# Kernel tuning notes

Hardware: AMD Instinct MI355X
Metric: run time of the kernel (lower is better)

## Reference

```python
import jax, jax.numpy as jnp
import numpy as np

BLOCK = 64
THRESH = 0.95
EPS = 1e-8


def setup_inputs() -> dict:
    key = jax.random.key(0)
    kq, kk, kv = jax.random.split(key, 3)
    S, D = 4096, 128
    q = jax.random.normal(kq, (S, D), dtype=jnp.float32)
    k = jax.random.normal(kk, (S, D), dtype=jnp.float32)
    v = jax.random.normal(kv, (S, D), dtype=jnp.float32)
    return {"q": q, "k": k, "v": v}


def reference(q, k, v):
    S, D = q.shape
    nb = S // BLOCK
    qb = q.reshape(nb, BLOCK, D)
    kb = k.reshape(nb, BLOCK, D)
    vb = v.reshape(nb, BLOCK, D)
    # all block-pair scores: [nb_q, nb_k, BLOCK_q, BLOCK_k]
    scores = jnp.einsum('ibd,jcd->ijbc', qb, kb)
    m = jnp.max(scores, axis=-1, keepdims=True)
    e = jnp.exp(scores - m)
    s = jnp.sum(e, axis=-1, keepdims=True)  # per-block-pair softmax denominator
    # top-p truncation mask: sort descending, cumsum, threshold
    srt = jnp.sort(e, axis=-1)[..., ::-1]
    cum = jnp.cumsum(srt, axis=-1)
    mask = cum < THRESH * s
    # NOTE: faithful to original — mask (in sorted order) is applied to the
    # UNSORTED exp_scores, exactly as the torch code does (indices unused).
    em = e * mask
    em = em / (jnp.sum(em, axis=-1, keepdims=True) + EPS)
    # accumulate over key blocks j (per-pair normalized weights, summed)
    out = jnp.einsum('ijbc,jcd->ibd', em, vb)
    return out.reshape(S, D)
```

## Files before the change

### kernel.cpp

```cpp
#include <hip/hip_runtime.h>
#include <cstdint>
#include <cstddef>


#define SEQ   4096
#define DIM   128
#define BLK   64
#define NB    (SEQ / BLK)
#define NJG   16
#define JPB   (NB / NJG)
#define NT    256
#define PSTR  12288
#define THRESH 0.95f
#define EPSF   1e-8f

typedef __attribute__((ext_vector_type(8))) _Float16 f16x8;
typedef __attribute__((ext_vector_type(4))) float    f32x4;

#define MFMAH(a, b, c) __builtin_amdgcn_mfma_f32_16x16x32_f16((a), (b), (c), 0, 0, 0)

union UH4 { uint2 u; _Float16 h[4]; };
union UH8 { uint4 u; f16x8 v; };

__device__ __forceinline__ void gll16(const uint* g, uint* l) {
  __builtin_amdgcn_global_load_lds(
      (const __attribute__((address_space(1))) void*)g,
      (__attribute__((address_space(3))) void*)l, 16, 0, 0);
}

__global__ __launch_bounds__(NT, 4) void eco_prep_kernel(
    const float* __restrict__ K, const float* __restrict__ V,
    uint* __restrict__ P, float* __restrict__ O) {
  const int tid  = threadIdx.x;
  const int b    = blockIdx.x;
  const int jb   = b >> 2;
  const int part = b & 3;

  {
    float4 z = {0.f, 0.f, 0.f, 0.f};
    float4* op = (float4*)O;
#pragma unroll
    for (int it = 0; it < 2; ++it) op[b * 512 + it * NT + tid] = z;
  }

  {
    const float4* gk = (const float4*)(K + (size_t)jb * BLK * DIM);
    uint* dst = P + (size_t)jb * PSTR;
#pragma unroll
    for (int it = 0; it < 2; ++it) {
      int f = part * 512 + it * NT + tid;
      int r = f >> 5, c4 = f & 31;
      float4 x = gk[f];
      float xs[4] = {x.x, x.y, x.z, x.w};
      UH4 uh, ur;
#pragma unroll
      for (int e = 0; e < 4; ++e) {
        float v = xs[e];
        _Float16 h = (_Float16)v;
        uh.h[e] = h;
        ur.h[e] = (_Float16)(v - (float)h);
      }
      uint off = (uint)r * 64u + (((uint)(c4 >> 1) ^ (uint)(r & 15)) << 2) +
                 (uint)((c4 & 1) << 1);
      *(uint2*)&dst[off]        = uh.u;
      *(uint2*)&dst[4096 + off] = ur.u;
    }
  }

  {
    const float* gv = V + (size_t)jb * BLK * DIM;
    uint4* dv = (uint4*)(P + (size_t)jb * PSTR + 8192);
    int idx = part * 256 + tid;
    int ch = idx >> 7, d = idx & 127;
    UH8 u;
#pragma unroll
    for (int j = 0; j < 8; ++j)
      u.v[j] = (_Float16)gv[(ch * 8 + j) * DIM + d];
    dv[idx] = u.u;
  }
}

#define CE(x, y, dmax) { float _hi = fmaxf((x), (y)); float _lo = fminf((x), (y)); \
                         (x) = (dmax) ? _hi : _lo; (y) = (dmax) ? _lo : _hi; }

__global__ __launch_bounds__(NT, 4) void eco_attn_kernel(
    const float* __restrict__ Q, const uint* __restrict__ P,
    float* __restrict__ O) {
  __shared__ __align__(16) uint sK[8192];
  __shared__ __align__(16) uint sW[2048];

  const int tid  = threadIdx.x;
  const int ib   = blockIdx.y;
  const int jg   = blockIdx.x;
  const int lane = tid & 63;
  const int wv   = tid >> 6;
  const int quad = lane >> 4;
  const int l16  = lane & 15;
  const int q4   = quad << 2;

  uint* sWw = sW + wv * 512;

  f16x8 qh[4], qr[4];
  {
    const float* qp = Q + (size_t)(ib * BLK + wv * 16 + l16) * DIM + quad * 8;
#pragma unroll
    for (int ks = 0; ks < 4; ++ks) {
      float4 x0 = *(const float4*)(qp + ks * 32);
      float4 x1 = *(const float4*)(qp + ks * 32 + 4);
      float xs[8] = {x0.x, x0.y, x0.z, x0.w, x1.x, x1.y, x1.z, x1.w};
      f16x8 h8, r8;
#pragma unroll
      for (int e = 0; e < 8; ++e) {
        float v = xs[e];
        _Float16 h = (_Float16)v;
        h8[e] = h;
        r8[e] = (_Float16)(v - (float)h);
      }
      qh[ks] = h8; qr[ks] = r8;
    }
  }

  const f32x4 zf = {0.f, 0.f, 0.f, 0.f};
  f32x4 pv[8];
#pragma unroll
  for (int i = 0; i < 8; ++i) pv[i] = zf;

  {
    const uint* gsrc = P + (size_t)(jg * JPB) * PSTR;
#pragma unroll
    for (int it = 0; it < 8; ++it) {
      int idx = (it * NT + tid) << 2;
      gll16(gsrc + idx, sK + idx);
    }
  }

  for (int jj = 0; jj < JPB; ++jj) {
    const int jb = jg * JPB + jj;
    __syncthreads();

    f32x4 ah[4], ar[4];
#pragma unroll
    for (int nt = 0; nt < 4; ++nt) { ah[nt] = zf; ar[nt] = zf; }
#pragma unroll
    for (int nt = 0; nt < 4; ++nt) {
      const int rB = nt * 16 + l16;
      const uint rowoff = (uint)rB * 64u;
      const uint swk = (uint)(rB & 15);
#pragma unroll
      for (int ks = 0; ks < 4; ++ks) {
        uint off = rowoff + ((((uint)(ks * 4 + quad)) ^ swk) << 2);
        f16x8 bh = *(const f16x8*)&sK[off];
        f16x8 br = *(const f16x8*)&sK[4096 + off];
        ah[nt] = MFMAH(bh, qh[ks], ah[nt]);
        ar[nt] = MFMAH(br, qh[ks], ar[nt]);
        ar[nt] = MFMAH(bh, qr[ks], ar[nt]);
      }
    }
    __syncthreads();

    if (jj + 1 < JPB) {
      const uint* gsrc = P + (size_t)(jb + 1) * PSTR;
#pragma unroll
      for (int it = 0; it < 8; ++it) {
        int idx = (it * NT + tid) << 2;
        gll16(gsrc + idx, sK + idx);
      }
    }

    {
      float a[16], e[16];
#pragma unroll
      for (int nt = 0; nt < 4; ++nt) {
        f32x4 s = ah[nt] + ar[nt];
#pragma unroll
        for (int rg = 0; rg < 4; ++rg) a[nt * 4 + rg] = s[rg];
      }
      float mt[8];
#pragma unroll
      for (int i = 0; i < 8; ++i) mt[i] = fmaxf(a[i], a[i + 8]);
#pragma unroll
      for (int w2 = 4; w2 >= 1; w2 >>= 1)
#pragma unroll
        for (int i = 0; i < w2; ++i) mt[i] = fmaxf(mt[i], mt[i + w2]);
      float m = mt[0];
      m = fmaxf(m, __shfl_xor(m, 16, 64));
      m = fmaxf(m, __shfl_xor(m, 32, 64));
#pragma unroll
      for (int i = 0; i < 16; ++i) { a[i] = __expf(a[i] - m); e[i] = a[i]; }
      float st[8];
#pragma unroll
      for (int i = 0; i < 8; ++i) st[i] = a[i] + a[i + 8];
#pragma unroll
      for (int w2 = 4; w2 >= 1; w2 >>= 1)
#pragma unroll
        for (int i = 0; i < w2; ++i) st[i] += st[i + w2];
      float sr = st[0];
      sr += __shfl_xor(sr, 16, 64);
      sr += __shfl_xor(sr, 32, 64);
      const float T = THRESH * sr;

      const int s = quad;
#pragma unroll
      for (int k2 = 2; k2 <= 8; k2 <<= 1)
#pragma unroll
        for (int j2 = k2 >> 1; j2 >= 1; j2 >>= 1)
#pragma unroll
          for (int i = 0; i < 16; ++i) {
            int l = i ^ j2;
            if (l > i) { bool d = ((i & k2) == 0); CE(a[i], a[l], d); }
          }
      const bool x16 = ((s & 1) == 0);
      const bool x32 = ((s & 2) == 0);
#pragma unroll
      for (int j2 = 8; j2 >= 1; j2 >>= 1)
#pragma unroll
        for (int i = 0; i < 16; ++i) {
          int l = i ^ j2;
          if (l > i) { CE(a[i], a[l], x16); }
        }
      {
        const bool km = (x32 == x16);
#pragma unroll
        for (int i = 0; i < 16; ++i) {
          float o = __shfl_xor(a[i], 16, 64);
          a[i] = km ? fmaxf(a[i], o) : fminf(a[i], o);
        }
#pragma unroll
        for (int j2 = 8; j2 >= 1; j2 >>= 1)
#pragma unroll
          for (int i = 0; i < 16; ++i) {
            int l = i ^ j2;
            if (l > i) { CE(a[i], a[l], x32); }
          }
      }
      {
#pragma unroll
        for (int i = 0; i < 16; ++i) {
          float o = __shfl_xor(a[i], 32, 64);
          a[i] = x32 ? fmaxf(a[i], o) : fminf(a[i], o);
        }
#pragma unroll
        for (int i = 0; i < 16; ++i) {
          float o = __shfl_xor(a[i], 16, 64);
          a[i] = x16 ? fmaxf(a[i], o) : fminf(a[i], o);
        }
#pragma unroll
        for (int j2 = 8; j2 >= 1; j2 >>= 1)
#pragma unroll
          for (int i = 0; i < 16; ++i) {
            int l = i ^ j2;
            if (l > i) { CE(a[i], a[l], true); }
          }
      }
#pragma unroll
      for (int i = 1; i < 16; ++i) a[i] += a[i - 1];
      float tot = a[15];
      float c = tot;
      float o1 = __shfl_up(c, 16, 64); if (s >= 1) c += o1;
      float o2 = __shfl_up(c, 32, 64); if (s >= 2) c += o2;
      const float excl = c - tot;
      int cnt = 0;
#pragma unroll
      for (int i = 0; i < 16; ++i) cnt += ((a[i] + excl) < T) ? 1 : 0;
      cnt += __shfl_xor(cnt, 16, 64);
      cnt += __shfl_xor(cnt, 32, 64);
      const int t = cnt;
      float p = 0.f;
#pragma unroll
      for (int i = 0; i < 16; ++i) {
        int kidx = ((i >> 2) << 4) + q4 + (i & 3);
        p += (kidx < t) ? e[i] : 0.f;
      }
      p += __shfl_xor(p, 16, 64);
      p += __shfl_xor(p, 32, 64);
      const float rn = 1.0f / (p + EPSF);
      uint* wrow = sWw + l16 * 32;
#pragma unroll
      for (int nt = 0; nt < 4; ++nt) {
        UH4 u;
#pragma unroll
        for (int rg = 0; rg < 4; ++rg) {
          int kidx = nt * 16 + q4 + rg;
          float w = (kidx < t) ? e[nt * 4 + rg] * rn : 0.f;
          u.h[rg] = (_Float16)w;
        }
        uint c4 = (uint)(nt * 4 + quad);
        *(uint2*)&wrow[(c4 ^ (uint)l16) << 1] = u.u;
      }
    }
    __builtin_amdgcn_wave_barrier();

    f16x8 wf[2];
#pragma unroll
    for (int ks2 = 0; ks2 < 2; ++ks2) {
      uint c0 = (uint)(ks2 * 8 + quad * 2);
      const uint* wrow = sWw + l16 * 32;
      uint2 lo = *(const uint2*)&wrow[(c0 ^ (uint)l16) << 1];
      uint2 hi = *(const uint2*)&wrow[((c0 + 1) ^ (uint)l16) << 1];
      UH8 u;
      u.u = make_uint4(lo.x, lo.y, hi.x, hi.y);
      wf[ks2] = u.v;
    }
    {
      const uint* gvt = P + (size_t)jb * PSTR + 8192;
#pragma unroll
      for (int nt2 = 0; nt2 < 8; ++nt2) {
#pragma unroll
        for (int ks2 = 0; ks2 < 2; ++ks2) {
          f16x8 vf = *(const f16x8*)&gvt[((uint)((ks2 * 4 + quad) * 128 +
                                                 nt2 * 16 + l16)) << 2];
          pv[nt2] = MFMAH(wf[ks2], vf, pv[nt2]);
        }
      }
    }
  }

#pragma unroll
  for (int nt2 = 0; nt2 < 8; ++nt2) {
    const int col  = nt2 * 16 + l16;
    const int row0 = ib * BLK + wv * 16 + quad * 4;
#pragma unroll
    for (int rg = 0; rg < 4; ++rg)
      atomicAdd(O + (size_t)(row0 + rg) * DIM + col, pv[nt2][rg]);
  }
}

extern "C" void kernel_launch(void* const* d_in, const int* in_sizes, int n_in,
                              void* d_out, int out_size, void* d_ws, size_t ws_size,
                              hipStream_t stream) {
  (void)in_sizes; (void)n_in; (void)ws_size; (void)out_size;
  const float* q = (const float*)d_in[0];
  const float* k = (const float*)d_in[1];
  const float* v = (const float*)d_in[2];
  float* out = (float*)d_out;
  uint* prep = (uint*)d_ws;

  eco_prep_kernel<<<dim3(NB * 4), dim3(NT), 0, stream>>>(k, v, prep, out);
  eco_attn_kernel<<<dim3(NJG, NB), dim3(NT), 0, stream>>>(q, prep, out);
}
```

Baseline: 119.0 us.

## Read K fragments directly from global memory, drop LDS staging, double split

Removes the shared-memory staging of K (global_load_lds plus two block barriers per key block) and instead has each wave load its MFMA K fragments straight from global memory. The prep kernel now writes K in a fragment-major layout so each lane's 16-byte load is contiguous. The key-block split doubles (NJG 16→32) and launch bounds request 8 blocks per CU, since LDS use drops to the per-wave weight buffer. The cost is more global/L2 traffic per block, because each block re-reads K from cache, and twice as many atomic adds into the output.

Result: slower. 188.7 us (+58.7%).

```diff
diff --git a/kernel.cpp b/kernel.cpp
--- a/kernel.cpp
+++ b/kernel.cpp
@@ -7,7 +7,7 @@
 #define DIM   128
 #define BLK   64
 #define NB    (SEQ / BLK)
-#define NJG   16
+#define NJG   32
 #define JPB   (NB / NJG)
 #define NT    256
 #define PSTR  12288
@@ -21,12 +21,6 @@
 
 union UH4 { uint2 u; _Float16 h[4]; };
 union UH8 { uint4 u; f16x8 v; };
-
-__device__ __forceinline__ void gll16(const uint* g, uint* l) {
-  __builtin_amdgcn_global_load_lds(
-      (const __attribute__((address_space(1))) void*)g,
-      (__attribute__((address_space(3))) void*)l, 16, 0, 0);
-}
 
 __global__ __launch_bounds__(NT, 4) void eco_prep_kernel(
     const float* __restrict__ K, const float* __restrict__ V,
@@ -44,27 +38,22 @@
   }
 
   {
-    const float4* gk = (const float4*)(K + (size_t)jb * BLK * DIM);
-    uint* dst = P + (size_t)jb * PSTR;
-#pragma unroll
-    for (int it = 0; it < 2; ++it) {
-      int f = part * 512 + it * NT + tid;
-      int r = f >> 5, c4 = f & 31;
-      float4 x = gk[f];
-      float xs[4] = {x.x, x.y, x.z, x.w};
-      UH4 uh, ur;
-#pragma unroll
-      for (int e = 0; e < 4; ++e) {
-        float v = xs[e];
-        _Float16 h = (_Float16)v;
-        uh.h[e] = h;
-        ur.h[e] = (_Float16)(v - (float)h);
-      }
-      uint off = (uint)r * 64u + (((uint)(c4 >> 1) ^ (uint)(r & 15)) << 2) +
-                 (uint)((c4 & 1) << 1);
-      *(uint2*)&dst[off]        = uh.u;
-      *(uint2*)&dst[4096 + off] = ur.u;
-    }
+    const float* gk = K + (size_t)jb * BLK * DIM;
+    uint4* dh = (uint4*)(P + (size_t)jb * PSTR);
+    uint4* dr = (uint4*)(P + (size_t)jb * PSTR + 4096);
+    int fi = part * 256 + tid;
+    int rB = fi & 63, kq = fi >> 6;
+    const float* src = gk + rB * DIM + kq * 8;
+    UH8 uh, ur;
+#pragma unroll
+    for (int j = 0; j < 8; ++j) {
+      float v = src[j];
+      _Float16 h = (_Float16)v;
+      uh.v[j] = h;
+      ur.v[j] = (_Float16)(v - (float)h);
+    }
+    dh[fi] = uh.u;
+    dr[fi] = ur.u;
   }
 
   {
@@ -83,10 +72,9 @@
 #define CE(x, y, dmax) { float _hi = fmaxf((x), (y)); float _lo = fminf((x), (y)); \
                          (x) = (dmax) ? _hi : _lo; (y) = (dmax) ? _lo : _hi; }
 
-__global__ __launch_bounds__(NT, 4) void eco_attn_kernel(
+__global__ __launch_bounds__(NT, 8) void eco_attn_kernel(
     const float* __restrict__ Q, const uint* __restrict__ P,
     float* __restrict__ O) {
-  __shared__ __align__(16) uint sK[8192];
   __shared__ __align__(16) uint sW[2048];
 
   const int tid  = threadIdx.x;
@@ -125,45 +113,25 @@
 #pragma unroll
   for (int i = 0; i < 8; ++i) pv[i] = zf;
 
-  {
-    const uint* gsrc = P + (size_t)(jg * JPB) * PSTR;
-#pragma unroll
-    for (int it = 0; it < 8; ++it) {
-      int idx = (it * NT + tid) << 2;
-      gll16(gsrc + idx, sK + idx);
-    }
-  }
-
   for (int jj = 0; jj < JPB; ++jj) {
     const int jb = jg * JPB + jj;
-    __syncthreads();
+    const uint* kf  = P + (size_t)jb * PSTR;
+    const uint* kfr = kf + 4096;
+    const uint* gvt = kf + 8192;
 
     f32x4 ah[4], ar[4];
 #pragma unroll
     for (int nt = 0; nt < 4; ++nt) { ah[nt] = zf; ar[nt] = zf; }
 #pragma unroll
     for (int nt = 0; nt < 4; ++nt) {
-      const int rB = nt * 16 + l16;
-      const uint rowoff = (uint)rB * 64u;
-      const uint swk = (uint)(rB & 15);
 #pragma unroll
       for (int ks = 0; ks < 4; ++ks) {
-        uint off = rowoff + ((((uint)(ks * 4 + quad)) ^ swk) << 2);
-        f16x8 bh = *(const f16x8*)&sK[off];
-        f16x8 br = *(const f16x8*)&sK[4096 + off];
+        uint fi = ((uint)((ks * 4 + quad) * 64 + nt * 16 + l16)) << 2;
+        f16x8 bh = *(const f16x8*)&kf[fi];
+        f16x8 br = *(const f16x8*)&kfr[fi];
         ah[nt] = MFMAH(bh, qh[ks], ah[nt]);
         ar[nt] = MFMAH(br, qh[ks], ar[nt]);
         ar[nt] = MFMAH(bh, qr[ks], ar[nt]);
-      }
-    }
-    __syncthreads();
-
-    if (jj + 1 < JPB) {
-      const uint* gsrc = P + (size_t)(jb + 1) * PSTR;
-#pragma unroll
-      for (int it = 0; it < 8; ++it) {
-        int idx = (it * NT + tid) << 2;
-        gll16(gsrc + idx, sK + idx);
       }
     }
 
@@ -301,18 +269,16 @@
       u.u = make_uint4(lo.x, lo.y, hi.x, hi.y);
       wf[ks2] = u.v;
     }
-    {
-      const uint* gvt = P + (size_t)jb * PSTR + 8192;
-#pragma unroll
-      for (int nt2 = 0; nt2 < 8; ++nt2) {
-#pragma unroll
-        for (int ks2 = 0; ks2 < 2; ++ks2) {
-          f16x8 vf = *(const f16x8*)&gvt[((uint)((ks2 * 4 + quad) * 128 +
-                                                 nt2 * 16 + l16)) << 2];
-          pv[nt2] = MFMAH(wf[ks2], vf, pv[nt2]);
-        }
-      }
-    }
+#pragma unroll
+    for (int nt2 = 0; nt2 < 8; ++nt2) {
+#pragma unroll
+      for (int ks2 = 0; ks2 < 2; ++ks2) {
+        f16x8 vf = *(const f16x8*)&gvt[((uint)((ks2 * 4 + quad) * 128 +
+                                               nt2 * 16 + l16)) << 2];
+        pv[nt2] = MFMAH(wf[ks2], vf, pv[nt2]);
+      }
+    }
+    __builtin_amdgcn_wave_barrier();
   }
 
 #pragma unroll
```

## Replace full bitonic sort with iterative max-extraction for top-p cutoff count

Applied to the files above, without the earlier changes.

Instead of bitonic-sorting the 64 exp scores per row across registers and lanes, the kernel repeatedly extracts the current maximum, accumulates it, and stops once the running sum reaches the threshold. Only the count of kept elements is needed, so the full sort is avoided when the cutoff is reached after few extractions, with an early exit once every row in the wave is done. With random inputs the 0.95 mass cutoff may need many of the 64 elements, so the loop can run close to its full length, and each step costs a reduction plus two shuffles. Tied values are all removed in one step, which can shift the count slightly compared with the sort.

After: 121.1 us. About the same (+1.8%).

```diff
diff --git a/kernel.cpp b/kernel.cpp
--- a/kernel.cpp
+++ b/kernel.cpp
@@ -28,6 +28,29 @@
       (__attribute__((address_space(3))) void*)l, 16, 0, 0);
 }
 
+__device__ __forceinline__ void ext_step(float (&w)[16], float& R, int& c,
+                                         bool& done, float T) {
+  float lt[8];
+#pragma unroll
+  for (int i = 0; i < 8; ++i) lt[i] = fmaxf(w[i], w[i + 8]);
+#pragma unroll
+  for (int w2 = 4; w2 >= 1; w2 >>= 1)
+#pragma unroll
+    for (int i = 0; i < w2; ++i) lt[i] = fmaxf(lt[i], lt[i + w2]);
+  const float lm = lt[0];
+  float v = fmaxf(lm, __shfl_xor(lm, 16, 64));
+  v = fmaxf(v, __shfl_xor(v, 32, 64));
+  const float cum = R + v;
+  const bool take = (!done) && (cum < T);
+  c += take ? 1 : 0;
+  if ((!done) && (lm == v)) {
+#pragma unroll
+    for (int i = 0; i < 16; ++i) w[i] = (w[i] == v) ? -1.0f : w[i];
+  }
+  R = done ? R : cum;
+  done = done || (cum >= T);
+}
+
 __global__ __launch_bounds__(NT, 4) void eco_prep_kernel(
     const float* __restrict__ K, const float* __restrict__ V,
     uint* __restrict__ P, float* __restrict__ O) {
@@ -79,9 +102,6 @@
     dv[idx] = u.u;
   }
 }
-
-#define CE(x, y, dmax) { float _hi = fmaxf((x), (y)); float _lo = fminf((x), (y)); \
-                         (x) = (dmax) ? _hi : _lo; (y) = (dmax) ? _lo : _hi; }
 
 __global__ __launch_bounds__(NT, 4) void eco_attn_kernel(
     const float* __restrict__ Q, const uint* __restrict__ P,
@@ -168,16 +188,16 @@
     }
 
     {
-      float a[16], e[16];
+      float e[16], w[16];
 #pragma unroll
       for (int nt = 0; nt < 4; ++nt) {
         f32x4 s = ah[nt] + ar[nt];
 #pragma unroll
-        for (int rg = 0; rg < 4; ++rg) a[nt * 4 + rg] = s[rg];
+        for (int rg = 0; rg < 4; ++rg) w[nt * 4 + rg] = s[rg];
       }
       float mt[8];
 #pragma unroll
-      for (int i = 0; i < 8; ++i) mt[i] = fmaxf(a[i], a[i + 8]);
+      for (int i = 0; i < 8; ++i) mt[i] = fmaxf(w[i], w[i + 8]);
 #pragma unroll
       for (int w2 = 4; w2 >= 1; w2 >>= 1)
 #pragma unroll
@@ -186,10 +206,10 @@
       m = fmaxf(m, __shfl_xor(m, 16, 64));
       m = fmaxf(m, __shfl_xor(m, 32, 64));
 #pragma unroll
-      for (int i = 0; i < 16; ++i) { a[i] = __expf(a[i] - m); e[i] = a[i]; }
+      for (int i = 0; i < 16; ++i) { w[i] = __expf(w[i] - m); e[i] = w[i]; }
       float st[8];
 #pragma unroll
-      for (int i = 0; i < 8; ++i) st[i] = a[i] + a[i + 8];
+      for (int i = 0; i < 8; ++i) st[i] = w[i] + w[i + 8];
 #pragma unroll
       for (int w2 = 4; w2 >= 1; w2 >>= 1)
 #pragma unroll
@@ -199,72 +219,17 @@
       sr += __shfl_xor(sr, 32, 64);
       const float T = THRESH * sr;
 
-      const int s = quad;
-#pragma unroll
-      for (int k2 = 2; k2 <= 8; k2 <<= 1)
-#pragma unroll
-        for (int j2 = k2 >> 1; j2 >= 1; j2 >>= 1)
-#pragma unroll
-          for (int i = 0; i < 16; ++i) {
-            int l = i ^ j2;
-            if (l > i) { bool d = ((i & k2) == 0); CE(a[i], a[l], d); }
-          }
-      const bool x16 = ((s & 1) == 0);
-      const bool x32 = ((s & 2) == 0);
-#pragma unroll
-      for (int j2 = 8; j2 >= 1; j2 >>= 1)
-#pragma unroll
-        for (int i = 0; i < 16; ++i) {
-          int l = i ^ j2;
-          if (l > i) { CE(a[i], a[l], x16); }
-        }
-      {
-        const bool km = (x32 == x16);
-#pragma unroll
-        for (int i = 0; i < 16; ++i) {
-          float o = __shfl_xor(a[i], 16, 64);
-          a[i] = km ? fmaxf(a[i], o) : fminf(a[i], o);
-        }
-#pragma unroll
-        for (int j2 = 8; j2 >= 1; j2 >>= 1)
-#pragma unroll
-          for (int i = 0; i < 16; ++i) {
-            int l = i ^ j2;
-            if (l > i) { CE(a[i], a[l], x32); }
-          }
-      }
-      {
-#pragma unroll
-        for (int i = 0; i < 16; ++i) {
-          float o = __shfl_xor(a[i], 32, 64);
-          a[i] = x32 ? fmaxf(a[i], o) : fminf(a[i], o);
-        }
-#pragma unroll
-        for (int i = 0; i < 16; ++i) {
-          float o = __shfl_xor(a[i], 16, 64);
-          a[i] = x16 ? fmaxf(a[i], o) : fminf(a[i], o);
-        }
-#pragma unroll
-        for (int j2 = 8; j2 >= 1; j2 >>= 1)
-#pragma unroll
-          for (int i = 0; i < 16; ++i) {
-            int l = i ^ j2;
-            if (l > i) { CE(a[i], a[l], true); }
-          }
-      }
-#pragma unroll
-      for (int i = 1; i < 16; ++i) a[i] += a[i - 1];
-      float tot = a[15];
-      float c = tot;
-      float o1 = __shfl_up(c, 16, 64); if (s >= 1) c += o1;
-      float o2 = __shfl_up(c, 32, 64); if (s >= 2) c += o2;
-      const float excl = c - tot;
-      int cnt = 0;
-#pragma unroll
-      for (int i = 0; i < 16; ++i) cnt += ((a[i] + excl) < T) ? 1 : 0;
-      cnt += __shfl_xor(cnt, 16, 64);
-      cnt += __shfl_xor(cnt, 32, 64);
-      const int t = cnt;
+      float R = 0.f;
+      int c = 0;
+      bool done = false;
+      ext_step(w, R, c, done, T);
+      ext_step(w, R, c, done, T);
+      ext_step(w, R, c, done, T);
+      ext_step(w, R, c, done, T);
+      for (int s2 = 0; s2 < 60 && __any(!done); ++s2)
+        ext_step(w, R, c, done, T);
+      const int t = c;
+
       float p = 0.f;
 #pragma unroll
       for (int i = 0; i < 16; ++i) {
@@ -281,8 +246,8 @@
 #pragma unroll
         for (int rg = 0; rg < 4; ++rg) {
           int kidx = nt * 16 + q4 + rg;
-          float w = (kidx < t) ? e[nt * 4 + rg] * rn : 0.f;
-          u.h[rg] = (_Float16)w;
+          float wgt = (kidx < t) ? e[nt * 4 + rg] * rn : 0.f;
+          u.h[rg] = (_Float16)wgt;
         }
         uint c4 = (uint)(nt * 4 + quad);
         *(uint2*)&wrow[(c4 ^ (uint)l16) << 1] = u.u;
@@ -313,6 +278,7 @@
         }
       }
     }
+    __builtin_amdgcn_wave_barrier();
   }
 
 #pragma unroll
```

## Stage only K-hi in LDS, read K-residual from global, use 24 uneven key groups

Applied to the files above, without the earlier changes.

Only the high fp16 half of each key block is staged in shared memory; the residual half is rewritten by the prep kernel into a fragment-contiguous layout and read straight from global memory. This halves the key staging buffer, so launch bounds rise from 4 to 6 blocks per CU. The key-block groups change from 16 groups of 4 to 24 uneven groups (sixteen of 3 and eight of 2), giving more blocks with fewer atomic-add rounds each. The trade-off is extra global/L2 traffic for the residual loads, load imbalance between groups, and more atomic contention on the output.

Result: slower. 182.8 us (+53.7%).

```diff
diff --git a/kernel.cpp b/kernel.cpp
--- a/kernel.cpp
+++ b/kernel.cpp
@@ -7,8 +7,7 @@
 #define DIM   128
 #define BLK   64
 #define NB    (SEQ / BLK)
-#define NJG   16
-#define JPB   (NB / NJG)
+#define NJG   24
 #define NT    256
 #define PSTR  12288
 #define THRESH 0.95f
@@ -45,7 +44,8 @@
 
   {
     const float4* gk = (const float4*)(K + (size_t)jb * BLK * DIM);
-    uint* dst = P + (size_t)jb * PSTR;
+    uint* dh = P + (size_t)jb * PSTR;
+    uint* dr = dh + 4096;
 #pragma unroll
     for (int it = 0; it < 2; ++it) {
       int f = part * 512 + it * NT + tid;
@@ -60,10 +60,12 @@
         uh.h[e] = h;
         ur.h[e] = (_Float16)(v - (float)h);
       }
-      uint off = (uint)r * 64u + (((uint)(c4 >> 1) ^ (uint)(r & 15)) << 2) +
-                 (uint)((c4 & 1) << 1);
-      *(uint2*)&dst[off]        = uh.u;
-      *(uint2*)&dst[4096 + off] = ur.u;
+      uint offh = (uint)r * 64u + (((uint)(c4 >> 1) ^ (uint)(r & 15)) << 2) +
+                  (uint)((c4 & 1) << 1);
+      uint offr = ((((uint)(c4 >> 1)) * 64u + (uint)r) << 2) +
+                  (uint)((c4 & 1) << 1);
+      *(uint2*)&dh[offh] = uh.u;
+      *(uint2*)&dr[offr] = ur.u;
     }
   }
 
@@ -83,10 +85,10 @@
 #define CE(x, y, dmax) { float _hi = fmaxf((x), (y)); float _lo = fminf((x), (y)); \
                          (x) = (dmax) ? _hi : _lo; (y) = (dmax) ? _lo : _hi; }
 
-__global__ __launch_bounds__(NT, 4) void eco_attn_kernel(
+__global__ __launch_bounds__(NT, 6) void eco_attn_kernel(
     const float* __restrict__ Q, const uint* __restrict__ P,
     float* __restrict__ O) {
-  __shared__ __align__(16) uint sK[8192];
+  __shared__ __align__(16) uint sK[4096];
   __shared__ __align__(16) uint sW[2048];
 
   const int tid  = threadIdx.x;
@@ -98,6 +100,9 @@
   const int l16  = lane & 15;
   const int q4   = quad << 2;
 
+  const int jb0 = (jg < 16) ? (3 * jg) : (48 + 2 * (jg - 16));
+  const int nj  = (jg < 16) ? 3 : 2;
+
   uint* sWw = sW + wv * 512;
 
   f16x8 qh[4], qr[4];
@@ -126,16 +131,18 @@
   for (int i = 0; i < 8; ++i) pv[i] = zf;
 
   {
-    const uint* gsrc = P + (size_t)(jg * JPB) * PSTR;
-#pragma unroll
-    for (int it = 0; it < 8; ++it) {
+    const uint* gsrc = P + (size_t)jb0 * PSTR;
+#pragma unroll
+    for (int it = 0; it < 4; ++it) {
       int idx = (it * NT + tid) << 2;
       gll16(gsrc + idx, sK + idx);
     }
   }
 
-  for (int jj = 0; jj < JPB; ++jj) {
-    const int jb = jg * JPB + jj;
+  for (int jj = 0; jj < nj; ++jj) {
+    const int jb = jb0 + jj;
+    const uint* kr  = P + (size_t)jb * PSTR + 4096;
+    const uint* gvt = P + (size_t)jb * PSTR + 8192;
     __syncthreads();
 
     f32x4 ah[4], ar[4];
@@ -150,7 +157,7 @@
       for (int ks = 0; ks < 4; ++ks) {
         uint off = rowoff + ((((uint)(ks * 4 + quad)) ^ swk) << 2);
         f16x8 bh = *(const f16x8*)&sK[off];
-        f16x8 br = *(const f16x8*)&sK[4096 + off];
+        f16x8 br = *(const f16x8*)&kr[((uint)((ks * 4 + quad) * 64 + rB)) << 2];
         ah[nt] = MFMAH(bh, qh[ks], ah[nt]);
         ar[nt] = MFMAH(br, qh[ks], ar[nt]);
         ar[nt] = MFMAH(bh, qr[ks], ar[nt]);
@@ -158,10 +165,10 @@
     }
     __syncthreads();
 
-    if (jj + 1 < JPB) {
+    if (jj + 1 < nj) {
       const uint* gsrc = P + (size_t)(jb + 1) * PSTR;
 #pragma unroll
-      for (int it = 0; it < 8; ++it) {
+      for (int it = 0; it < 4; ++it) {
         int idx = (it * NT + tid) << 2;
         gll16(gsrc + idx, sK + idx);
       }
@@ -281,8 +288,8 @@
 #pragma unroll
         for (int rg = 0; rg < 4; ++rg) {
           int kidx = nt * 16 + q4 + rg;
-          float w = (kidx < t) ? e[nt * 4 + rg] * rn : 0.f;
-          u.h[rg] = (_Float16)w;
+          float wgt = (kidx < t) ? e[nt * 4 + rg] * rn : 0.f;
+          u.h[rg] = (_Float16)wgt;
         }
         uint c4 = (uint)(nt * 4 + quad);
         *(uint2*)&wrow[(c4 ^ (uint)l16) << 1] = u.u;
@@ -301,18 +308,16 @@
       u.u = make_uint4(lo.x, lo.y, hi.x, hi.y);
       wf[ks2] = u.v;
     }
-    {
-      const uint* gvt = P + (size_t)jb * PSTR + 8192;
-#pragma unroll
-      for (int nt2 = 0; nt2 < 8; ++nt2) {
-#pragma unroll
-        for (int ks2 = 0; ks2 < 2; ++ks2) {
-          f16x8 vf = *(const f16x8*)&gvt[((uint)((ks2 * 4 + quad) * 128 +
-                                                 nt2 * 16 + l16)) << 2];
-          pv[nt2] = MFMAH(wf[ks2], vf, pv[nt2]);
-        }
-      }
-    }
+#pragma unroll
+    for (int nt2 = 0; nt2 < 8; ++nt2) {
+#pragma unroll
+      for (int ks2 = 0; ks2 < 2; ++ks2) {
+        f16x8 vf = *(const f16x8*)&gvt[((uint)((ks2 * 4 + quad) * 128 +
+                                               nt2 * 16 + l16)) << 2];
+        pv[nt2] = MFMAH(wf[ks2], vf, pv[nt2]);
+      }
+    }
+    __builtin_amdgcn_wave_barrier();
   }
 
 #pragma unroll
```
